# Performance work log

Hardware: AMD Instinct MI355X
Metric: run time of the kernel (lower is better)

Reference implementation:

```python
import jax, jax.numpy as jnp
import numpy as np

BLANK_LOGPROB = -1.0
NEG = -1e30  # finite stand-in for -inf (safe in fp32/bf16, differentiable masking)


def setup_inputs() -> dict:
    key = jax.random.key(0)
    k1, k2, k3 = jax.random.split(key, 3)
    B, T, L = 64, 2000, 400
    attn_logprob = jax.random.normal(k1, (B, 1, T, L), dtype=jnp.float32)
    # guarantee mel_len >= 2*text_len + 1 so the CTC path is always feasible
    text_lens = jax.random.randint(k2, (B,), 100, L + 1, dtype=jnp.int32)
    mel_lens = jax.random.randint(k3, (B,), 1000, T + 1, dtype=jnp.int32)
    return {"attn_logprob": attn_logprob, "text_lens": text_lens, "mel_lens": mel_lens}


def reference(attn_logprob, text_lens, mel_lens):
    B, _, T, L = attn_logprob.shape
    x = attn_logprob[:, 0]                                            # [B, T, L]
    # pad a blank class at index 0 along the text dim (pad=(1,0) in torch)
    x = jnp.pad(x, ((0, 0), (0, 0), (1, 0)), constant_values=BLANK_LOGPROB)
    # NOTE: the original log-softmaxes the FULL (unsliced) padded tensor
    lp = jax.nn.log_softmax(x, axis=-1)                               # [B, T, L+1]

    # CTC with targets = [1..text_len] (all distinct), blank = 0.
    # Extended label sequence: blank, 1, blank, 2, ..., blank, L, blank -> S = 2L+1
    S = 2 * L + 1
    s = jnp.arange(S)
    lab = jnp.where(s % 2 == 0, 0, s // 2 + 1)                        # [S] class id per ext pos
    is_label = (s % 2 == 1)                                           # skip transition allowed (no repeats)
    valid = s[None, :] < (2 * text_lens[:, None] + 1)                 # [B, S]

    neg = jnp.asarray(NEG, lp.dtype)
    emit = jnp.take(lp, lab, axis=2)                                  # [B, T, S]
    emit = jnp.where(valid[:, None, :], emit, neg)
    emits = jnp.swapaxes(emit, 0, 1)                                  # [T, B, S]

    alpha0 = jnp.where(s[None, :] < 2, emits[0], neg)                 # [B, S]

    def shift(a, k):
        return jnp.concatenate([jnp.full((B, k), neg, a.dtype), a[:, :S - k]], axis=1)

    def step(alpha, xs):
        e_t, t = xs
        stacked = jnp.stack(
            [alpha,
             shift(alpha, 1),
             jnp.where(is_label[None, :], shift(alpha, 2), neg)], axis=0)
        new = e_t + jax.scipy.special.logsumexp(stacked, axis=0)
        # freeze alpha once past this sample's input length
        new = jnp.where((t < mel_lens)[:, None], new, alpha)
        return new, None

    alpha, _ = jax.lax.scan(step, alpha0, (emits[1:], jnp.arange(1, T)))

    end = jnp.stack([2 * text_lens, 2 * text_lens - 1], axis=1)       # [B, 2]
    a_end = jnp.take_along_axis(alpha, end, axis=1)
    logalpha = jax.scipy.special.logsumexp(a_end, axis=1)             # [B]
    # torch CTCLoss(reduction='mean') divides each sample by target_length;
    # the module then averages over batch. zero_infinity -> zero out infinite losses.
    loss = -logalpha / text_lens.astype(lp.dtype)
    loss = jnp.where(logalpha > NEG / 2, loss, jnp.zeros_like(loss))
    return jnp.mean(loss)
```

## Files before the change

kernel.cpp:

```cpp
#include <hip/hip_runtime.h>
#include <math.h>


namespace {
constexpr int kB = 64;
constexpr int kT = 2000;
constexpr int kL = 400;
constexpr int kC = 16;
constexpr int kRow = 408;
constexpr float kEblank = 0.36787944117144233f;
}

__global__ __launch_bounds__(256, 1) void ctc_forward_kernel(
        const float* __restrict__ attn, const int* __restrict__ text_lens,
        const int* __restrict__ mel_lens, float* __restrict__ loss_ws) {
    __shared__ __align__(16) float wbuf[2][kC][kRow];
    __shared__ float psum[2][kC * 100];
    __shared__ double sLd;

    const int b    = blockIdx.x;
    const int tid  = threadIdx.x;
    const int lane = tid & 63;
    const int wv   = tid >> 6;
    const int Lb = text_lens[b];
    const int Tb = mel_lens[b];
    const int Sb = 2 * Lb + 1;
    const int nck = (Tb + kC - 1) / kC;

    const float4* __restrict__ rp4 = (const float4*)(attn + (size_t)b * kT * kL);

    {
        const int slot = tid >> 7, row = (tid >> 3) & 15, j = tid & 7;
        wbuf[slot][row][400 + j] = 0.f;
    }

    const int pid = tid - 64;
    float4 rgE[9], rgO[9];

    auto load_chunk = [&](int ck, float4 (&rg)[9]) {
        const int t0 = ck * kC;
        #pragma unroll
        for (int i = 0; i < 9; ++i) {
            const int task = pid + 192 * i;
            if (task < kC * 100) {
                const int r = task / 100, q = task - r * 100;
                if (t0 + r < Tb) rg[i] = rp4[(size_t)(t0 + r) * 100 + q];
            }
        }
    };
    auto store_chunk = [&](int ck, const float4 (&rg)[9]) {
        const int slot = ck & 1;
        const int t0 = ck * kC;
        #pragma unroll
        for (int i = 0; i < 9; ++i) {
            const int task = pid + 192 * i;
            if (task < kC * 100) {
                const int r = task / 100, q = task - r * 100;
                float s4 = 0.f;
                if (t0 + r < Tb) {
                    const float4 x = rg[i];
                    const float e0 = __expf(x.x), e1 = __expf(x.y);
                    const float e2 = __expf(x.z), e3 = __expf(x.w);
                    s4 = (e0 + e1) + (e2 + e3);
                    const int l0 = 4 * q;
                    float4 w4;
                    w4.x = (l0 + 0 < Lb) ? e0 : 0.f;
                    w4.y = (l0 + 1 < Lb) ? e1 : 0.f;
                    w4.z = (l0 + 2 < Lb) ? e2 : 0.f;
                    w4.w = (l0 + 3 < Lb) ? e3 : 0.f;
                    *(float4*)&wbuf[slot][r][4 * q] = w4;
                }
                psum[slot][task] = s4;
            }
        }
    };

    double Ld = 0.0;
    auto reduce_lse = [&](int ck) {
        const int ps = ck & 1;
        const int r = lane >> 2, k = lane & 3;
        float s = 0.f;
        #pragma unroll
        for (int m = 0; m < 25; ++m) s += psum[ps][r * 100 + k + 4 * m];
        s += __shfl_xor(s, 1);
        s += __shfl_xor(s, 2);
        float lv = (k == 0 && (ck * kC + r) < Tb) ? __logf(s + kEblank) : 0.f;
        lv += __shfl_xor(lv, 4);
        lv += __shfl_xor(lv, 8);
        lv += __shfl_xor(lv, 16);
        lv += __shfl_xor(lv, 32);
        Ld += (double)lv;
    };

    const int gi  = (lane < 50) ? lane : 50;
    const int bpa = ((lane - 1) & 63) << 2;
    float a[16];
    #pragma unroll
    for (int i = 0; i < 16; ++i) a[i] = 0.f;
    double Ct = 0.0;
    float red = 1.0f;

    auto step = [&](const float* __restrict__ wr) {
        float w[8];
        *(float4*)&w[0] = *(const float4*)(wr);
        *(float4*)&w[4] = *(const float4*)(wr + 4);
        const float p1 = __int_as_float(
            __builtin_amdgcn_ds_bpermute(bpa, __float_as_int(a[15])));
        float n[16];
        {
            const float s = a[0] + p1;
            n[0] = kEblank * s;
            n[1] = w[0] * (a[1] + s);
        }
        #pragma unroll
        for (int j = 1; j < 8; ++j) {
            const float s = a[2 * j] + a[2 * j - 1];
            n[2 * j]     = kEblank * s;
            n[2 * j + 1] = w[j] * (a[2 * j + 1] + s);
        }
        #pragma unroll
        for (int i = 0; i < 16; ++i) a[i] = n[i];
    };
    auto fold = [&]() {
        const float tot = red;
        const float c = 1.0f / tot;
        Ct += (double)__logf(tot);
        float ns = 0.f;
        #pragma unroll
        for (int i = 0; i < 16; ++i) { a[i] *= c; ns += a[i]; }
        red = ns;
    };
    auto consumer_chunk = [&](int ck) {
        const float* wr = &wbuf[ck & 1][0][8 * gi];
        if (ck == 0) {
            if (lane == 0) { a[0] = kEblank; a[1] = wbuf[0][0][0]; }
            #pragma unroll
            for (int r = 1; r < kC; ++r) step(wr + r * kRow);
            fold();
        } else if (ck < nck - 1) {
            step(wr);             red += __shfl_xor(red, 1);
            step(wr + kRow);      red += __shfl_xor(red, 2);
            step(wr + 2 * kRow);  red += __shfl_xor(red, 4);
            step(wr + 3 * kRow);  red += __shfl_xor(red, 8);
            step(wr + 4 * kRow);  red += __shfl_xor(red, 16);
            step(wr + 5 * kRow);  red += __shfl_xor(red, 32);
            #pragma unroll
            for (int r = 6; r < kC; ++r) step(wr + r * kRow);
            fold();
        } else {
            const int t0 = ck * kC;
            for (int r = 0; r < kC; ++r) {
                if (t0 + r >= Tb) break;
                step(wr + r * kRow);
            }
        }
    };

    if (wv > 0) {
        load_chunk(0, rgE);
        store_chunk(0, rgE);
        load_chunk(1, rgO);
    }
    __syncthreads();

    for (int ck = 0; ck < nck; ck += 2) {
        if (wv == 0) {
            consumer_chunk(ck);
        } else {
            if (ck + 1 < nck) store_chunk(ck + 1, rgO);
            load_chunk(ck + 2, rgE);
            if (wv == 1) reduce_lse(ck);
        }
        __syncthreads();
        if (ck + 1 < nck) {
            if (wv == 0) {
                consumer_chunk(ck + 1);
            } else {
                if (ck + 2 < nck) store_chunk(ck + 2, rgE);
                load_chunk(ck + 3, rgO);
                if (wv == 1) reduce_lse(ck + 1);
            }
            __syncthreads();
        }
    }

    float* afin = (float*)wbuf;
    if (wv == 0 && lane <= 50) {
        #pragma unroll
        for (int i = 0; i < 16; ++i) afin[16 * lane + i] = a[i];
    }
    if (wv == 1 && lane == 0) sLd = Ld;
    __syncthreads();
    if (tid == 0) {
        const float tail = afin[Sb - 2] + afin[Sb - 1];
        const double la = (double)__logf(tail) + Ct - sLd;
        float loss = 0.f;
        if (la > -5e29) loss = (float)(-la / (double)Lb);
        loss_ws[b] = loss;
    }
}

__global__ void mean64_kernel(const float* __restrict__ loss_ws,
                              float* __restrict__ out) {
    float v = loss_ws[threadIdx.x];
    #pragma unroll
    for (int off = 32; off > 0; off >>= 1) v += __shfl_xor(v, off);
    if (threadIdx.x == 0) out[0] = v * (1.0f / 64.0f);
}

extern "C" void kernel_launch(void* const* d_in, const int* in_sizes, int n_in,
                              void* d_out, int out_size, void* d_ws, size_t ws_size,
                              hipStream_t stream) {
    const float* attn      = (const float*)d_in[0];
    const int*   text_lens = (const int*)d_in[1];
    const int*   mel_lens  = (const int*)d_in[2];
    float* loss_ws = (float*)d_ws;

    ctc_forward_kernel<<<kB, 256, 0, stream>>>(attn, text_lens, mel_lens, loss_ws);
    mean64_kernel<<<1, 64, 0, stream>>>(loss_ws, (float*)d_out);
}
```

Baseline: 547.5 us.

## Reformulate CTC recurrence in blank/label state pairs with software-pipelined emit loads

```diff
diff --git a/kernel.cpp b/kernel.cpp
--- a/kernel.cpp
+++ b/kernel.cpp
@@ -24,7 +24,6 @@
     const int wv   = tid >> 6;
     const int Lb = text_lens[b];
     const int Tb = mel_lens[b];
-    const int Sb = 2 * Lb + 1;
     const int nck = (Tb + kC - 1) / kC;
 
     const float4* __restrict__ rp4 = (const float4*)(attn + (size_t)b * kT * kL);
@@ -94,64 +93,104 @@
 
     const int gi  = (lane < 50) ? lane : 50;
     const int bpa = ((lane - 1) & 63) << 2;
-    float a[16];
+    float u[8], o[8];
     #pragma unroll
-    for (int i = 0; i < 16; ++i) a[i] = 0.f;
+    for (int i = 0; i < 8; ++i) { u[i] = 0.f; o[i] = 0.f; }
     double Ct = 0.0;
     float red = 1.0f;
-
-    auto step = [&](const float* __restrict__ wr) {
-        float w[8];
-        *(float4*)&w[0] = *(const float4*)(wr);
-        *(float4*)&w[4] = *(const float4*)(wr + 4);
-        const float p1 = __int_as_float(
-            __builtin_amdgcn_ds_bpermute(bpa, __float_as_int(a[15])));
-        float n[16];
-        {
-            const float s = a[0] + p1;
-            n[0] = kEblank * s;
-            n[1] = w[0] * (a[1] + s);
-        }
-        #pragma unroll
-        for (int j = 1; j < 8; ++j) {
-            const float s = a[2 * j] + a[2 * j - 1];
-            n[2 * j]     = kEblank * s;
-            n[2 * j + 1] = w[j] * (a[2 * j + 1] + s);
-        }
-        #pragma unroll
-        for (int i = 0; i < 16; ++i) a[i] = n[i];
-    };
+    float wA[8], wB[8];
+
+#define LOADW(W, PTR)                                  \
+    {                                                  \
+        *(float4*)&W[0] = *(const float4*)(PTR);       \
+        *(float4*)&W[4] = *(const float4*)((PTR) + 4); \
+    }
+
+#define STEP_UO(WC, WN, NPTR, DOLOAD)                                    \
+    {                                                                    \
+        const float op7 = WC[7] * (o[7] + u[7]);                         \
+        const float p = __int_as_float(                                  \
+            __builtin_amdgcn_ds_bpermute(bpa, __float_as_int(op7)));     \
+        if (DOLOAD) LOADW(WN, NPTR);                                     \
+        const float op0 = WC[0] * (o[0] + u[0]);                         \
+        const float op1 = WC[1] * (o[1] + u[1]);                         \
+        const float op2 = WC[2] * (o[2] + u[2]);                         \
+        const float op3 = WC[3] * (o[3] + u[3]);                         \
+        const float op4 = WC[4] * (o[4] + u[4]);                         \
+        const float op5 = WC[5] * (o[5] + u[5]);                         \
+        const float op6 = WC[6] * (o[6] + u[6]);                         \
+        u[7] = __builtin_fmaf(kEblank, u[7], op6);                       \
+        u[6] = __builtin_fmaf(kEblank, u[6], op5);                       \
+        u[5] = __builtin_fmaf(kEblank, u[5], op4);                       \
+        u[4] = __builtin_fmaf(kEblank, u[4], op3);                       \
+        u[3] = __builtin_fmaf(kEblank, u[3], op2);                       \
+        u[2] = __builtin_fmaf(kEblank, u[2], op1);                       \
+        u[1] = __builtin_fmaf(kEblank, u[1], op0);                       \
+        u[0] = __builtin_fmaf(kEblank, u[0], p);                         \
+        o[0] = op0; o[1] = op1; o[2] = op2; o[3] = op3;                  \
+        o[4] = op4; o[5] = op5; o[6] = op6; o[7] = op7;                  \
+    }
+
     auto fold = [&]() {
         const float tot = red;
         const float c = 1.0f / tot;
         Ct += (double)__logf(tot);
         float ns = 0.f;
         #pragma unroll
-        for (int i = 0; i < 16; ++i) { a[i] *= c; ns += a[i]; }
+        for (int i = 0; i < 8; ++i) {
+            u[i] *= c; o[i] *= c;
+            ns += u[i] + o[i];
+        }
         red = ns;
     };
+
     auto consumer_chunk = [&](int ck) {
         const float* wr = &wbuf[ck & 1][0][8 * gi];
         if (ck == 0) {
-            if (lane == 0) { a[0] = kEblank; a[1] = wbuf[0][0][0]; }
-            #pragma unroll
-            for (int r = 1; r < kC; ++r) step(wr + r * kRow);
+            if (lane == 0) { u[0] = kEblank; o[0] = wbuf[0][0][0]; }
+            LOADW(wA, wr + kRow);
+            STEP_UO(wA, wB, wr + 2 * kRow, 1)
+            STEP_UO(wB, wA, wr + 3 * kRow, 1)
+            STEP_UO(wA, wB, wr + 4 * kRow, 1)
+            STEP_UO(wB, wA, wr + 5 * kRow, 1)
+            STEP_UO(wA, wB, wr + 6 * kRow, 1)
+            STEP_UO(wB, wA, wr + 7 * kRow, 1)
+            STEP_UO(wA, wB, wr + 8 * kRow, 1)
+            STEP_UO(wB, wA, wr + 9 * kRow, 1)
+            STEP_UO(wA, wB, wr + 10 * kRow, 1)
+            STEP_UO(wB, wA, wr + 11 * kRow, 1)
+            STEP_UO(wA, wB, wr + 12 * kRow, 1)
+            STEP_UO(wB, wA, wr + 13 * kRow, 1)
+            STEP_UO(wA, wB, wr + 14 * kRow, 1)
+            STEP_UO(wB, wA, wr + 15 * kRow, 1)
+            STEP_UO(wA, wB, wr, 0)
             fold();
         } else if (ck < nck - 1) {
-            step(wr);             red += __shfl_xor(red, 1);
-            step(wr + kRow);      red += __shfl_xor(red, 2);
-            step(wr + 2 * kRow);  red += __shfl_xor(red, 4);
-            step(wr + 3 * kRow);  red += __shfl_xor(red, 8);
-            step(wr + 4 * kRow);  red += __shfl_xor(red, 16);
-            step(wr + 5 * kRow);  red += __shfl_xor(red, 32);
-            #pragma unroll
-            for (int r = 6; r < kC; ++r) step(wr + r * kRow);
+            LOADW(wA, wr);
+            STEP_UO(wA, wB, wr + 1 * kRow, 1)  red += __shfl_xor(red, 1);
+            STEP_UO(wB, wA, wr + 2 * kRow, 1)  red += __shfl_xor(red, 2);
+            STEP_UO(wA, wB, wr + 3 * kRow, 1)  red += __shfl_xor(red, 4);
+            STEP_UO(wB, wA, wr + 4 * kRow, 1)  red += __shfl_xor(red, 8);
+            STEP_UO(wA, wB, wr + 5 * kRow, 1)  red += __shfl_xor(red, 16);
+            STEP_UO(wB, wA, wr + 6 * kRow, 1)  red += __shfl_xor(red, 32);
+            STEP_UO(wA, wB, wr + 7 * kRow, 1)
+            STEP_UO(wB, wA, wr + 8 * kRow, 1)
+            STEP_UO(wA, wB, wr + 9 * kRow, 1)
+            STEP_UO(wB, wA, wr + 10 * kRow, 1)
+            STEP_UO(wA, wB, wr + 11 * kRow, 1)
+            STEP_UO(wB, wA, wr + 12 * kRow, 1)
+            STEP_UO(wA, wB, wr + 13 * kRow, 1)
+            STEP_UO(wB, wA, wr + 14 * kRow, 1)
+            STEP_UO(wA, wB, wr + 15 * kRow, 1)
+            STEP_UO(wB, wA, wr, 0)
             fold();
         } else {
             const int t0 = ck * kC;
             for (int r = 0; r < kC; ++r) {
                 if (t0 + r >= Tb) break;
-                step(wr + r * kRow);
+                const float* ww = wr + r * kRow;
+                LOADW(wA, ww);
+                STEP_UO(wA, wB, ww, 0)
             }
         }
     };
@@ -167,8 +206,8 @@
         if (wv == 0) {
             consumer_chunk(ck);
         } else {
+            load_chunk(ck + 2, rgE);
             if (ck + 1 < nck) store_chunk(ck + 1, rgO);
-            load_chunk(ck + 2, rgE);
             if (wv == 1) reduce_lse(ck);
         }
         __syncthreads();
@@ -176,8 +215,8 @@
             if (wv == 0) {
                 consumer_chunk(ck + 1);
             } else {
+                load_chunk(ck + 3, rgO);
                 if (ck + 2 < nck) store_chunk(ck + 2, rgE);
-                load_chunk(ck + 3, rgO);
                 if (wv == 1) reduce_lse(ck + 1);
             }
             __syncthreads();
@@ -187,17 +226,19 @@
     float* afin = (float*)wbuf;
     if (wv == 0 && lane <= 50) {
         #pragma unroll
-        for (int i = 0; i < 16; ++i) afin[16 * lane + i] = a[i];
+        for (int i = 0; i < 8; ++i) afin[8 * lane + i] = u[i];
     }
     if (wv == 1 && lane == 0) sLd = Ld;
     __syncthreads();
     if (tid == 0) {
-        const float tail = afin[Sb - 2] + afin[Sb - 1];
+        const float tail = afin[Lb];
         const double la = (double)__logf(tail) + Ct - sLd;
         float loss = 0.f;
         if (la > -5e29) loss = (float)(-la / (double)Lb);
         loss_ws[b] = loss;
     }
+#undef STEP_UO
+#undef LOADW
 }
 
 __global__ void mean64_kernel(const float* __restrict__ loss_ws,
```

New measurement: 847.5 us. +54.8%, slower.

## Restructure CTC recurrence into blank/label state arrays with early bpermute

Applied to the files above, without the earlier changes.

```diff
diff --git a/kernel.cpp b/kernel.cpp
--- a/kernel.cpp
+++ b/kernel.cpp
@@ -24,7 +24,6 @@
     const int wv   = tid >> 6;
     const int Lb = text_lens[b];
     const int Tb = mel_lens[b];
-    const int Sb = 2 * Lb + 1;
     const int nck = (Tb + kC - 1) / kC;
 
     const float4* __restrict__ rp4 = (const float4*)(attn + (size_t)b * kT * kL);
@@ -94,32 +93,35 @@
 
     const int gi  = (lane < 50) ? lane : 50;
     const int bpa = ((lane - 1) & 63) << 2;
-    float a[16];
+    float u[8], o[8];
     #pragma unroll
-    for (int i = 0; i < 16; ++i) a[i] = 0.f;
+    for (int i = 0; i < 8; ++i) { u[i] = 0.f; o[i] = 0.f; }
     double Ct = 0.0;
     float red = 1.0f;
 
-    auto step = [&](const float* __restrict__ wr) {
-        float w[8];
-        *(float4*)&w[0] = *(const float4*)(wr);
-        *(float4*)&w[4] = *(const float4*)(wr + 4);
-        const float p1 = __int_as_float(
-            __builtin_amdgcn_ds_bpermute(bpa, __float_as_int(a[15])));
-        float n[16];
-        {
-            const float s = a[0] + p1;
-            n[0] = kEblank * s;
-            n[1] = w[0] * (a[1] + s);
-        }
-        #pragma unroll
-        for (int j = 1; j < 8; ++j) {
-            const float s = a[2 * j] + a[2 * j - 1];
-            n[2 * j]     = kEblank * s;
-            n[2 * j + 1] = w[j] * (a[2 * j + 1] + s);
-        }
-        #pragma unroll
-        for (int i = 0; i < 16; ++i) a[i] = n[i];
+    auto step = [&](const float* __restrict__ wr_row) {
+        const float4 wlo = *(const float4*)(wr_row);
+        const float4 whi = *(const float4*)(wr_row + 4);
+        const float op7 = whi.w * (o[7] + u[7]);
+        const float p = __int_as_float(
+            __builtin_amdgcn_ds_bpermute(bpa, __float_as_int(op7)));
+        const float op0 = wlo.x * (o[0] + u[0]);
+        const float op1 = wlo.y * (o[1] + u[1]);
+        const float op2 = wlo.z * (o[2] + u[2]);
+        const float op3 = wlo.w * (o[3] + u[3]);
+        const float op4 = whi.x * (o[4] + u[4]);
+        const float op5 = whi.y * (o[5] + u[5]);
+        const float op6 = whi.z * (o[6] + u[6]);
+        u[7] = __builtin_fmaf(kEblank, u[7], op6);
+        u[6] = __builtin_fmaf(kEblank, u[6], op5);
+        u[5] = __builtin_fmaf(kEblank, u[5], op4);
+        u[4] = __builtin_fmaf(kEblank, u[4], op3);
+        u[3] = __builtin_fmaf(kEblank, u[3], op2);
+        u[2] = __builtin_fmaf(kEblank, u[2], op1);
+        u[1] = __builtin_fmaf(kEblank, u[1], op0);
+        u[0] = __builtin_fmaf(kEblank, u[0], p);
+        o[0] = op0; o[1] = op1; o[2] = op2; o[3] = op3;
+        o[4] = op4; o[5] = op5; o[6] = op6; o[7] = op7;
     };
     auto fold = [&]() {
         const float tot = red;
@@ -127,13 +129,16 @@
         Ct += (double)__logf(tot);
         float ns = 0.f;
         #pragma unroll
-        for (int i = 0; i < 16; ++i) { a[i] *= c; ns += a[i]; }
+        for (int i = 0; i < 8; ++i) {
+            u[i] *= c; o[i] *= c;
+            ns += u[i] + o[i];
+        }
         red = ns;
     };
     auto consumer_chunk = [&](int ck) {
         const float* wr = &wbuf[ck & 1][0][8 * gi];
         if (ck == 0) {
-            if (lane == 0) { a[0] = kEblank; a[1] = wbuf[0][0][0]; }
+            if (lane == 0) { u[0] = kEblank; o[0] = wbuf[0][0][0]; }
             #pragma unroll
             for (int r = 1; r < kC; ++r) step(wr + r * kRow);
             fold();
@@ -187,12 +192,12 @@
     float* afin = (float*)wbuf;
     if (wv == 0 && lane <= 50) {
         #pragma unroll
-        for (int i = 0; i < 16; ++i) afin[16 * lane + i] = a[i];
+        for (int i = 0; i < 8; ++i) afin[8 * lane + i] = u[i];
     }
     if (wv == 1 && lane == 0) sLd = Ld;
     __syncthreads();
     if (tid == 0) {
-        const float tail = afin[Sb - 2] + afin[Sb - 1];
+        const float tail = afin[Lb];
         const double la = (double)__logf(tail) + Ct - sLd;
         float loss = 0.f;
         if (la > -5e29) loss = (float)(-la / (double)Lb);
```

New measurement: 801.2 us. 46.3% more time.
